# Kernel tuning notes

Hardware: AMD Instinct MI355X
Metric: run time of the kernel (lower is better)

## Reference

```python
import jax, jax.numpy as jnp
import numpy as np

REPLACE = 4
REMAIN = 32
EPS = 1e-12


def _l2norm(x, axis):
    return x / jnp.maximum(jnp.linalg.norm(x, axis=axis, keepdims=True), EPS)


def setup_inputs() -> dict:
    key = jax.random.key(0)
    ks = jax.random.split(key, 16)
    B, d = 4096, 64
    n_users, n_entities, n_items = 100000, 200000, 50000
    K, n_cans, n_rel = 64, 64, 100
    return {
        "users": jax.random.randint(ks[0], (B,), 0, n_users),
        "items": jax.random.randint(ks[1], (B,), 0, n_items),
        "kg_neighbors": jax.random.randint(ks[2], (n_items, K), 0, n_entities),
        "all_candidates": jax.random.randint(ks[3], (n_rel, n_cans), 0, n_entities),
        "neighbor_relations": jax.random.randint(ks[4], (n_items, K), 0, n_rel),
        "user_all_embeddings": jax.random.normal(ks[5], (n_users, d), jnp.float32),
        "entity_all_embeddings": jax.random.normal(ks[6], (n_entities, d), jnp.float32),
        "item_embeddings": jax.random.normal(ks[7], (B, d), jnp.float32),
        "ui_W": jax.random.normal(ks[8], (2 * d, d), jnp.float32) / np.sqrt(2 * d),
        "ui_b": jnp.zeros((d,), jnp.float32),
        "e1_W": jax.random.normal(ks[9], (d, d), jnp.float32) / np.sqrt(d),
        "e1_b": jnp.zeros((d,), jnp.float32),
        "e2_W": jax.random.normal(ks[10], (d, d), jnp.float32) / np.sqrt(d),
        "e2_b": jnp.zeros((d,), jnp.float32),
    }


def reference(users, items, kg_neighbors, all_candidates, neighbor_relations,
              user_all_embeddings, entity_all_embeddings, item_embeddings,
              ui_W, ui_b, e1_W, e1_b, e2_W, e2_b):
    B = users.shape[0]
    d = user_all_embeddings.shape[1]
    idx_dtype = kg_neighbors.dtype

    neighbors = kg_neighbors[items]                      # [B, K]
    users_e = user_all_embeddings[users]                 # [B, d]
    ui_e = _l2norm(jnp.concatenate([users_e, item_embeddings], axis=1) @ ui_W + ui_b, 1)  # [B, d]

    # Step 1: score neighbors, pick top replace_num
    ne = _l2norm(entity_all_embeddings[neighbors] @ e1_W + e1_b, 2)   # [B, K, d]
    scores1 = jnp.einsum('bd,bkd->bk', ui_e, ne)
    logits1 = jax.nn.softmax(scores1, axis=1)
    step1_prob, step1_idx = jax.lax.top_k(logits1, REPLACE)          # [B, R]
    replaced = jnp.take_along_axis(neighbors, step1_idx, axis=1)     # [B, R]
    sel_rel = jnp.take_along_axis(neighbor_relations[items], step1_idx, axis=1)
    cf_kg1 = kg_neighbors.at[items[:, None], step1_idx].set(
        jnp.zeros((B, REPLACE), idx_dtype))
    ap1 = jnp.log(jnp.mean(step1_prob, axis=1))                      # [B]

    # Step 2: candidate pruning + sampling
    cands = all_candidates[sel_rel]                                  # [B, R, C]
    cands_e = entity_all_embeddings[cands]                           # [B, R, C, d]
    scores2 = jnp.einsum('bd,brcd->brc', users_e, cands_e)
    _, remain_idx = jax.lax.top_k(scores2, REMAIN)                   # [B, R, M]
    cands = jnp.take_along_axis(cands, remain_idx, axis=2).reshape(B * REPLACE, REMAIN)

    replaced_e = _l2norm(entity_all_embeddings[replaced] @ e1_W + e1_b, 2)
    replaced_e = replaced_e.reshape(B * REPLACE, d)
    cands_e2 = _l2norm(entity_all_embeddings[cands] @ e2_W + e2_b, 2)  # [BR, M, d]
    ui_rep = jnp.repeat(ui_e, REPLACE, axis=0)                         # [BR, d]
    s2 = jnp.einsum('nd,nmd->nm', ui_rep * replaced_e, cands_e2)       # [BR, M]
    logp2 = jax.nn.log_softmax(s2, axis=1)

    skey = jax.random.key(42)
    step2_idx = jax.random.categorical(skey, logp2, axis=1)           # [BR]
    rows = jnp.arange(B * REPLACE)
    step2_prob = jnp.exp(logp2[rows, step2_idx]).reshape(B, REPLACE)
    sel_ent = cands[rows, step2_idx].reshape(B, REPLACE)
    cf_kg2 = kg_neighbors.at[items[:, None], step1_idx].set(sel_ent.astype(idx_dtype))
    ap2 = jnp.log(jnp.mean(step1_prob, axis=1)) + jnp.log(jnp.mean(step2_prob, axis=1))
    return (cf_kg1, ap1, cf_kg2, ap2)
```

## Files before the change

### kernel.cpp

```cpp
#include <hip/hip_runtime.h>
#include <stdint.h>

#define EPS_NORM 1e-12f
#define F32_TINY 1.17549435e-38f

static __device__ __forceinline__ int rfl(int v) {
  return __builtin_amdgcn_readfirstlane(v);
}

__device__ __forceinline__ void threefry2x32(uint32_t k0, uint32_t k1,
                                             uint32_t x0, uint32_t x1,
                                             uint32_t& o0, uint32_t& o1) {
  uint32_t ks2 = k0 ^ k1 ^ 0x1BD11BDAu;
  x0 += k0; x1 += k1;
#define TF_ROT(r) { x0 += x1; x1 = (x1 << (r)) | (x1 >> (32 - (r))); x1 ^= x0; }
  TF_ROT(13) TF_ROT(15) TF_ROT(26) TF_ROT(6)
  x0 += k1; x1 += ks2 + 1u;
  TF_ROT(17) TF_ROT(29) TF_ROT(16) TF_ROT(24)
  x0 += ks2; x1 += k0 + 2u;
  TF_ROT(13) TF_ROT(15) TF_ROT(26) TF_ROT(6)
  x0 += k0; x1 += k1 + 3u;
  TF_ROT(17) TF_ROT(29) TF_ROT(16) TF_ROT(24)
  x0 += k1; x1 += ks2 + 4u;
  TF_ROT(13) TF_ROT(15) TF_ROT(26) TF_ROT(6)
  x0 += ks2; x1 += k0 + 5u;
#undef TF_ROT
  o0 = x0; o1 = x1;
}

__global__ __launch_bounds__(256) void k_init(const int* __restrict__ kg,
                                              float* __restrict__ out0,
                                              int* __restrict__ wkg2, int n) {
  int i = blockIdx.x * 256 + threadIdx.x;
  if (i < n) { int v = kg[i]; out0[i] = (float)v; wkg2[i] = v; }
}

__device__ __forceinline__ void transform_row(const float4* __restrict__ Er,
                                              const float* __restrict__ W,
                                              const float* __restrict__ bias,
                                              float (&yn)[64]) {
  float y[64];
#pragma unroll
  for (int j = 0; j < 64; ++j) y[j] = 0.f;
  float4 c0 = Er[0], c1 = Er[1], c2 = Er[2], c3 = Er[3];
#pragma unroll 1
  for (int cc = 0; cc < 4; ++cc) {
    float4 n0, n1, n2, n3;
    if (cc < 3) { n0 = Er[cc * 4 + 4]; n1 = Er[cc * 4 + 5];
                  n2 = Er[cc * 4 + 6]; n3 = Er[cc * 4 + 7]; }
    float ev[16] = {c0.x, c0.y, c0.z, c0.w, c1.x, c1.y, c1.z, c1.w,
                    c2.x, c2.y, c2.z, c2.w, c3.x, c3.y, c3.z, c3.w};
#pragma unroll
    for (int k2i = 0; k2i < 16; ++k2i) {
      const float4* Wr = reinterpret_cast<const float4*>(
          W + ((size_t)(cc * 16 + k2i)) * 64);
      float ek = ev[k2i];
#pragma unroll
      for (int j4 = 0; j4 < 16; ++j4) {
        float4 w = Wr[j4];
        y[j4 * 4 + 0] = fmaf(ek, w.x, y[j4 * 4 + 0]);
        y[j4 * 4 + 1] = fmaf(ek, w.y, y[j4 * 4 + 1]);
        y[j4 * 4 + 2] = fmaf(ek, w.z, y[j4 * 4 + 2]);
        y[j4 * 4 + 3] = fmaf(ek, w.w, y[j4 * 4 + 3]);
      }
    }
    c0 = n0; c1 = n1; c2 = n2; c3 = n3;
  }
  const float4* B4 = reinterpret_cast<const float4*>(bias);
#pragma unroll
  for (int j4 = 0; j4 < 16; ++j4) {
    float4 bb = B4[j4];
    float bv[4] = {bb.x, bb.y, bb.z, bb.w};
#pragma unroll
    for (int t = 0; t < 4; ++t) y[j4 * 4 + t] = __fadd_rn(y[j4 * 4 + t], bv[t]);
  }
  float S1[32];
#pragma unroll
  for (int i = 0; i < 32; ++i)
    S1[i] = __fadd_rn(__fmul_rn(y[i], y[i]), __fmul_rn(y[i + 32], y[i + 32]));
#pragma unroll
  for (int i = 0; i < 16; ++i) S1[i] = __fadd_rn(S1[i], S1[i + 16]);
#pragma unroll
  for (int i = 0; i < 8; ++i)  S1[i] = __fadd_rn(S1[i], S1[i + 8]);
#pragma unroll
  for (int i = 0; i < 4; ++i)  S1[i] = __fadd_rn(S1[i], S1[i + 4]);
#pragma unroll
  for (int i = 0; i < 2; ++i)  S1[i] = __fadd_rn(S1[i], S1[i + 2]);
  float ss = __fadd_rn(S1[0], S1[1]);
  float denom = fmaxf(sqrtf(ss), EPS_NORM);
#pragma unroll
  for (int j = 0; j < 64; ++j) yn[j] = y[j] / denom;
}

__global__ __launch_bounds__(256) void k_tx(
    const float* __restrict__ E, const int* __restrict__ allc,
    const float* __restrict__ W1, const float* __restrict__ b1,
    const float* __restrict__ W2, const float* __restrict__ b2,
    float* __restrict__ T1, float* __restrict__ T2c,
    int nEnt , int nCand ) {
  int tid = threadIdx.x, wv = tid >> 6, lane = tid & 63;
  int w = rfl(blockIdx.x * 4 + wv);
  int wEnt = nEnt >> 6;
  int wTot = wEnt + (nCand >> 6);
  if (w >= wTot) return;
  const float *W, *bias; float* dst; int srow, drow;
  if (w < wEnt) { drow = w * 64 + lane; srow = drow; W = W1; bias = b1; dst = T1; }
  else { drow = (w - wEnt) * 64 + lane; srow = allc[drow]; W = W2; bias = b2; dst = T2c; }
  const float4* Er = reinterpret_cast<const float4*>(E + (size_t)srow * 64);
  float yn[64];
  transform_row(Er, W, bias, yn);
  float4* D4 = reinterpret_cast<float4*>(dst + (size_t)drow * 64);
#pragma unroll
  for (int j4 = 0; j4 < 16; ++j4)
    D4[j4] = make_float4(yn[4 * j4], yn[4 * j4 + 1], yn[4 * j4 + 2], yn[4 * j4 + 3]);
}

__global__ __launch_bounds__(256) void k_transform64(
    const float* __restrict__ src, const int* __restrict__ gidx,
    const float* __restrict__ W, const float* __restrict__ bias,
    float* __restrict__ out, int nrows) {
  __shared__ float Wl[4096];
  for (int i = threadIdx.x; i < 4096; i += 256) Wl[i] = W[i];
  __syncthreads();
  int wid = threadIdx.x >> 6, lane = threadIdx.x & 63;
  int row = rfl(blockIdx.x * 4 + wid);
  if (row >= nrows) return;
  int srow = rfl(gidx ? gidx[row] : row);
  const float* er = src + (size_t)srow * 64;
  float y = 0.f;
#pragma unroll
  for (int k = 0; k < 64; ++k) y = fmaf(er[k], Wl[k * 64 + lane], y);
  y += bias[lane];
  float ss = y * y;
#pragma unroll
  for (int off = 32; off; off >>= 1) ss += __shfl_xor(ss, off);
  float yn = y / fmaxf(sqrtf(ss), EPS_NORM);
  out[(size_t)row * 64 + lane] = yn;
}

__global__ __launch_bounds__(256) void k_ui(
    const float* __restrict__ U, const int* __restrict__ users,
    const float* __restrict__ Iemb, const float* __restrict__ W,
    const float* __restrict__ bias, float* __restrict__ out, int B) {
  __shared__ float Wl[8192];
  for (int i = threadIdx.x; i < 8192; i += 256) Wl[i] = W[i];
  __syncthreads();
  int wid = threadIdx.x >> 6, lane = threadIdx.x & 63;
  int b = rfl(blockIdx.x * 4 + wid);
  if (b >= B) return;
  int usr = rfl(users[b]);
  const float* ur = U + (size_t)usr * 64;
  const float* ir = Iemb + (size_t)b * 64;
  float y = 0.f;
#pragma unroll
  for (int k = 0; k < 64; ++k) y = fmaf(ur[k], Wl[k * 64 + lane], y);
#pragma unroll
  for (int k = 0; k < 64; ++k) y = fmaf(ir[k], Wl[(64 + k) * 64 + lane], y);
  y += bias[lane];
  float ss = y * y;
#pragma unroll
  for (int off = 32; off; off >>= 1) ss += __shfl_xor(ss, off);
  float yn = y / fmaxf(sqrtf(ss), EPS_NORM);
  out[(size_t)b * 64 + lane] = yn;
}

__device__ __forceinline__ void score1_tail(
    float s, int lane, int b, int item, int nb,
    const int* __restrict__ nrel,
    float* __restrict__ out0, float* __restrict__ ap1_out,
    int* __restrict__ s1_idx, int* __restrict__ s1_rel, int* __restrict__ s1_ent,
    float* __restrict__ lmp1) {
  float m = s;
#pragma unroll
  for (int off = 32; off; off >>= 1) m = fmaxf(m, __shfl_xor(m, off));
  float ex = expf(s - m);
  float sum = ex;
#pragma unroll
  for (int off = 32; off; off >>= 1) sum += __shfl_xor(sum, off);
  float p = ex / sum;
  int rank = 0;
  for (int k2 = 0; k2 < 64; ++k2) {
    float pv = __shfl(p, k2);
    rank += (pv > p || (pv == p && k2 < lane)) ? 1 : 0;
  }
  float acc = 0.f;
#pragma unroll
  for (int rr = 0; rr < 4; ++rr) {
    unsigned long long msk = __ballot(rank == rr);
    int src = __ffsll(msk) - 1;
    acc += __shfl(p, src);
  }
  float lm = logf(acc * 0.25f);
  if (lane == 0) { ap1_out[b] = lm; lmp1[b] = lm; }
  if (rank < 4) {
    s1_idx[b * 4 + rank] = lane;
    s1_ent[b * 4 + rank] = nb;
    s1_rel[b * 4 + rank] = nrel[(size_t)item * 64 + lane];
    out0[(size_t)item * 64 + lane] = 0.0f;
  }
}

__global__ __launch_bounds__(256) void k_score1g(
    const int* __restrict__ items, const int* __restrict__ kg,
    const int* __restrict__ nrel, const float* __restrict__ T1,
    const float* __restrict__ uiE,
    float* __restrict__ out0, float* __restrict__ ap1_out,
    int* __restrict__ s1_idx, int* __restrict__ s1_rel, int* __restrict__ s1_ent,
    float* __restrict__ lmp1) {
  int tid = threadIdx.x, wv = tid >> 6, lane = tid & 63;
  int b = rfl(blockIdx.x * 4 + wv);
  int item = rfl(items[b]);
  int nb = kg[(size_t)item * 64 + lane];
  const float4* R = reinterpret_cast<const float4*>(T1 + (size_t)nb * 64);
  float yn[64];
#pragma unroll
  for (int j4 = 0; j4 < 16; ++j4) {
    float4 v = R[j4];
    yn[4 * j4] = v.x; yn[4 * j4 + 1] = v.y; yn[4 * j4 + 2] = v.z; yn[4 * j4 + 3] = v.w;
  }
  const float4* Ur = reinterpret_cast<const float4*>(uiE + (size_t)b * 64);
  float D[32];
#pragma unroll
  for (int i4 = 0; i4 < 8; ++i4) {
    float4 ua = Ur[i4], ub = Ur[i4 + 8];
    float uav[4] = {ua.x, ua.y, ua.z, ua.w};
    float ubv[4] = {ub.x, ub.y, ub.z, ub.w};
#pragma unroll
    for (int t = 0; t < 4; ++t) {
      int i = i4 * 4 + t;
      D[i] = __fadd_rn(__fmul_rn(yn[i], uav[t]), __fmul_rn(yn[i + 32], ubv[t]));
    }
  }
#pragma unroll
  for (int i = 0; i < 16; ++i) D[i] = __fadd_rn(D[i], D[i + 16]);
#pragma unroll
  for (int i = 0; i < 8; ++i)  D[i] = __fadd_rn(D[i], D[i + 8]);
#pragma unroll
  for (int i = 0; i < 4; ++i)  D[i] = __fadd_rn(D[i], D[i + 4]);
#pragma unroll
  for (int i = 0; i < 2; ++i)  D[i] = __fadd_rn(D[i], D[i + 2]);
  float s = __fadd_rn(D[0], D[1]);
  score1_tail(s, lane, b, item, nb, nrel, out0, ap1_out, s1_idx, s1_rel, s1_ent, lmp1);
}

__global__ __launch_bounds__(256) void k_score1(
    const int* __restrict__ items, const int* __restrict__ kg,
    const int* __restrict__ nrel, const float* __restrict__ E,
    const float* __restrict__ W1, const float* __restrict__ b1,
    const float* __restrict__ uiE,
    float* __restrict__ out0, float* __restrict__ ap1_out,
    int* __restrict__ s1_idx, int* __restrict__ s1_rel, int* __restrict__ s1_ent,
    float* __restrict__ lmp1) {
  int tid = threadIdx.x, wv = tid >> 6, lane = tid & 63;
  int b = rfl(blockIdx.x * 4 + wv);
  int item = rfl(items[b]);
  int nb = kg[(size_t)item * 64 + lane];
  const float4* Er = reinterpret_cast<const float4*>(E + (size_t)nb * 64);
  float yn[64];
  transform_row(Er, W1, b1, yn);
  const float4* Ur = reinterpret_cast<const float4*>(uiE + (size_t)b * 64);
  float D[32];
#pragma unroll
  for (int i4 = 0; i4 < 8; ++i4) {
    float4 ua = Ur[i4], ub = Ur[i4 + 8];
    float uav[4] = {ua.x, ua.y, ua.z, ua.w};
    float ubv[4] = {ub.x, ub.y, ub.z, ub.w};
#pragma unroll
    for (int t = 0; t < 4; ++t) {
      int i = i4 * 4 + t;
      D[i] = __fadd_rn(__fmul_rn(yn[i], uav[t]), __fmul_rn(yn[i + 32], ubv[t]));
    }
  }
#pragma unroll
  for (int i = 0; i < 16; ++i) D[i] = __fadd_rn(D[i], D[i + 16]);
#pragma unroll
  for (int i = 0; i < 8; ++i)  D[i] = __fadd_rn(D[i], D[i + 8]);
#pragma unroll
  for (int i = 0; i < 4; ++i)  D[i] = __fadd_rn(D[i], D[i + 4]);
#pragma unroll
  for (int i = 0; i < 2; ++i)  D[i] = __fadd_rn(D[i], D[i + 2]);
  float s = __fadd_rn(D[0], D[1]);
  score1_tail(s, lane, b, item, nb, nrel, out0, ap1_out, s1_idx, s1_rel, s1_ent, lmp1);
}

__global__ __launch_bounds__(256) void k_score2(
    const int* __restrict__ users, const int* __restrict__ s1_rel,
    const float* __restrict__ U, const float* __restrict__ E,
    const int* __restrict__ allc, int* __restrict__ kept, int N) {
  int wid = threadIdx.x >> 6, lane = threadIdx.x & 63;
  int n = rfl(blockIdx.x * 4 + wid);
  if (n >= N) return;
  int b = n >> 2;
  int rel = rfl(s1_rel[n]);
  int usr = rfl(users[b]);
  int ent = allc[rel * 64 + lane];
  const float* ur = U + (size_t)usr * 64;
  const float4* e4 = reinterpret_cast<const float4*>(E + (size_t)ent * 64);
  float s = 0.f;
#pragma unroll
  for (int j4 = 0; j4 < 16; ++j4) {
    float4 t = e4[j4];
    s = fmaf(ur[4 * j4 + 0], t.x, s);
    s = fmaf(ur[4 * j4 + 1], t.y, s);
    s = fmaf(ur[4 * j4 + 2], t.z, s);
    s = fmaf(ur[4 * j4 + 3], t.w, s);
  }
  int rank = 0;
  for (int k2 = 0; k2 < 64; ++k2) {
    float sv = __shfl(s, k2);
    rank += (sv > s || (sv == s && k2 < lane)) ? 1 : 0;
  }
  if (rank < 32) kept[n * 32 + rank] = (lane << 18) | ent;
}

__device__ __forceinline__ void sample_body(
    float q, int n, int b, int lane,
    const int* __restrict__ items, const int* __restrict__ s1_idx,
    int rel, const float* __restrict__ T2c, const int* __restrict__ kept,
    float* __restrict__ p2, int* __restrict__ wkg2) {
  int m = lane & 31;
  int pk = kept[n * 32 + m];
  int c = pk >> 18;
  int ent = pk & 0x3FFFF;
  const float4* c4 = reinterpret_cast<const float4*>(T2c + ((size_t)rel * 64 + c) * 64);
  float s = 0.f;
#pragma unroll
  for (int j4 = 0; j4 < 16; ++j4) {
    float4 t = c4[j4];
    s = fmaf(__shfl(q, 4 * j4 + 0), t.x, s);
    s = fmaf(__shfl(q, 4 * j4 + 1), t.y, s);
    s = fmaf(__shfl(q, 4 * j4 + 2), t.z, s);
    s = fmaf(__shfl(q, 4 * j4 + 3), t.w, s);
  }
  float mx = s;
#pragma unroll
  for (int off = 1; off < 32; off <<= 1) mx = fmaxf(mx, __shfl_xor(mx, off));
  float shv = s - mx;
  float se = expf(shv);
  float sum = se;
#pragma unroll
  for (int off = 1; off < 32; off <<= 1) sum += __shfl_xor(sum, off);
  float logp = shv - logf(sum);
  uint32_t h0, h1;
  threefry2x32(0u, 42u, 0u, (uint32_t)(n * 32 + m), h0, h1);
  uint32_t bits = h0 ^ h1;
  float u0 = __uint_as_float((bits >> 9) | 0x3F800000u) - 1.0f;
  float uu = fmaxf(u0, F32_TINY);
  float g = -logf(-logf(uu));
  float z = g + logp;
  float bz = z; int bm = m;
#pragma unroll
  for (int off = 1; off < 32; off <<= 1) {
    float oz = __shfl_xor(bz, off);
    int om = __shfl_xor(bm, off);
    if (oz > bz || (oz == bz && om < bm)) { bz = oz; bm = om; }
  }
  if (lane == bm) {
    p2[n] = expf(logp);
    int col = s1_idx[n];
    int item = items[b];
    atomicMax(&wkg2[(size_t)item * 64 + col], ((b + 1) << 18) | ent);
  }
}

__global__ __launch_bounds__(256) void k_sample2(
    const int* __restrict__ items,
    const int* __restrict__ s1_idx, const int* __restrict__ s1_rel,
    const int* __restrict__ s1_ent, const float* __restrict__ T1,
    const float* __restrict__ T2c, const float* __restrict__ uiE,
    const int* __restrict__ kept,
    float* __restrict__ p2, int* __restrict__ wkg2, int N) {
  int tid = threadIdx.x, wid = tid >> 6, lane = tid & 63;
  int n = rfl(blockIdx.x * 4 + wid);
  if (n >= N) return;
  int b = n >> 2;
  int rel = rfl(s1_rel[n]);
  int repl = rfl(s1_ent[n]);
  float q = uiE[(size_t)b * 64 + lane] * T1[(size_t)repl * 64 + lane];
  sample_body(q, n, b, lane, items, s1_idx, rel, T2c, kept, p2, wkg2);
}

__global__ __launch_bounds__(256) void k_sample(
    const int* __restrict__ items,
    const int* __restrict__ s1_idx, const int* __restrict__ s1_rel,
    const int* __restrict__ s1_ent,
    const float* __restrict__ E, const float* __restrict__ W1,
    const float* __restrict__ b1, const float* __restrict__ T2c,
    const float* __restrict__ uiE, const int* __restrict__ kept,
    float* __restrict__ p2, int* __restrict__ wkg2, int N) {
  __shared__ float Wl[4096];
  int tid = threadIdx.x;
  for (int i = tid; i < 4096; i += 256) Wl[i] = W1[i];
  __syncthreads();
  int wid = tid >> 6, lane = tid & 63;
  int n = rfl(blockIdx.x * 4 + wid);
  if (n >= N) return;
  int b = n >> 2;
  int rel = rfl(s1_rel[n]);
  int repl = rfl(s1_ent[n]);
  const float* er = E + (size_t)repl * 64;
  float y = 0.f;
#pragma unroll
  for (int k2 = 0; k2 < 64; ++k2) y = fmaf(er[k2], Wl[k2 * 64 + lane], y);
  y += b1[lane];
  float ss = y * y;
#pragma unroll
  for (int off = 32; off; off >>= 1) ss += __shfl_xor(ss, off);
  float yn = y / fmaxf(sqrtf(ss), EPS_NORM);
  float q = uiE[(size_t)b * 64 + lane] * yn;
  sample_body(q, n, b, lane, items, s1_idx, rel, T2c, kept, p2, wkg2);
}

__global__ __launch_bounds__(256) void k_fin(const int* __restrict__ wkg2,
                                             const float* __restrict__ p2,
                                             const float* __restrict__ lmp1,
                                             float* __restrict__ out2,
                                             float* __restrict__ out3,
                                             int n, int B) {
  int i = blockIdx.x * 256 + threadIdx.x;
  if (i < n) out2[i] = (float)(wkg2[i] & 0x3FFFF);
  if (i < B) {
    float a = ((p2[i * 4] + p2[i * 4 + 1]) + p2[i * 4 + 2]) + p2[i * 4 + 3];
    out3[i] = lmp1[i] + logf(a * 0.25f);
  }
}

extern "C" void kernel_launch(void* const* d_in, const int* in_sizes, int n_in,
                              void* d_out, int out_size, void* d_ws, size_t ws_size,
                              hipStream_t stream) {
  const int*   users = (const int*)d_in[0];
  const int*   items = (const int*)d_in[1];
  const int*   kg    = (const int*)d_in[2];
  const int*   allc  = (const int*)d_in[3];
  const int*   nrel  = (const int*)d_in[4];
  const float* U     = (const float*)d_in[5];
  const float* E     = (const float*)d_in[6];
  const float* Iemb  = (const float*)d_in[7];
  const float* uiW   = (const float*)d_in[8];
  const float* uib   = (const float*)d_in[9];
  const float* e1W   = (const float*)d_in[10];
  const float* e1b   = (const float*)d_in[11];
  const float* e2W   = (const float*)d_in[12];
  const float* e2b   = (const float*)d_in[13];

  const int B = 4096, NCELL = 3200000, NCAND = 6400, NR4 = 16384, NENT = 200000;

  float* out0    = (float*)d_out;
  float* out_ap1 = out0 + NCELL;
  float* out2    = out_ap1 + B;
  float* out_ap2 = out2 + NCELL;

  float* T2c  = (float*)d_ws;
  float* uiE  = T2c + 409600;
  int*   wkg2 = (int*)(uiE + 262144);
  int*   s1i  = wkg2 + NCELL;
  int*   s1r  = s1i + NR4;
  int*   s1e  = s1r + NR4;
  int*   kept = s1e + NR4;
  float* p2   = (float*)(kept + 524288);
  float* lmp1 = p2 + NR4;
  float* T1   = lmp1 + B;
  const size_t WS_NEED = ((size_t)(T1 + (size_t)NENT * 64) - (size_t)d_ws);
  const bool pathA = ws_size >= WS_NEED;

  k_init<<<(NCELL + 255) / 256, 256, 0, stream>>>(kg, out0, wkg2, NCELL);
  k_ui<<<(B + 3) / 4, 256, 0, stream>>>(U, users, Iemb, uiW, uib, uiE, B);
  if (pathA) {
    int wTot = (NENT >> 6) + (NCAND >> 6);
    k_tx<<<(wTot + 3) / 4, 256, 0, stream>>>(E, allc, e1W, e1b, e2W, e2b,
                                             T1, T2c, NENT, NCAND);
    k_score1g<<<B / 4, 256, 0, stream>>>(items, kg, nrel, T1, uiE,
                                         out0, out_ap1, s1i, s1r, s1e, lmp1);
    k_score2<<<(NR4 + 3) / 4, 256, 0, stream>>>(users, s1r, U, E, allc, kept, NR4);
    k_sample2<<<(NR4 + 3) / 4, 256, 0, stream>>>(items, s1i, s1r, s1e, T1, T2c,
                                                 uiE, kept, p2, wkg2, NR4);
  } else {
    k_transform64<<<(NCAND + 3) / 4, 256, 0, stream>>>(E, allc, e2W, e2b, T2c, NCAND);
    k_score1<<<B / 4, 256, 0, stream>>>(items, kg, nrel, E, e1W, e1b, uiE,
                                        out0, out_ap1, s1i, s1r, s1e, lmp1);
    k_score2<<<(NR4 + 3) / 4, 256, 0, stream>>>(users, s1r, U, E, allc, kept, NR4);
    k_sample<<<(NR4 + 3) / 4, 256, 0, stream>>>(items, s1i, s1r, s1e, E, e1W, e1b,
                                                T2c, uiE, kept, p2, wkg2, NR4);
  }
  k_fin<<<(NCELL + 255) / 256, 256, 0, stream>>>(wkg2, p2, lmp1, out2, out_ap2,
                                                 NCELL, B);
}
```

Before: 158.6 us.

## Fuse init, ui, and entity transforms into one phase-1 kernel

Merges k_init, k_ui and k_tx into a single k_phase1 launch whose blocks are partitioned by role. The entity transform now stages W in LDS and has each lane compute one output column for four rows per pass, with a wave-shuffle norm, instead of one row per lane held in registers. The candidate embeddings are also gathered into a compact buffer (borrowed from the out2 region) so score2 reads them contiguously. The intent is fewer launches, lower register pressure and better memory locality, at the cost of fixed hardcoded block counts and reusing the output buffer as scratch.

```diff
diff --git a/kernel.cpp b/kernel.cpp
--- a/kernel.cpp
+++ b/kernel.cpp
@@ -28,6 +28,98 @@
   o0 = x0; o1 = x1;
 }
 
+__global__ __launch_bounds__(256) void k_phase1(
+    const float* __restrict__ E, const int* __restrict__ allc,
+    const float* __restrict__ W1, const float* __restrict__ b1,
+    const float* __restrict__ W2, const float* __restrict__ b2,
+    const float* __restrict__ U, const int* __restrict__ users,
+    const float* __restrict__ Iemb, const float* __restrict__ uiW,
+    const float* __restrict__ uib, const int* __restrict__ kg,
+    float* __restrict__ T1, float* __restrict__ T2c, float* __restrict__ Eg,
+    float* __restrict__ uiE, float* __restrict__ out0, int* __restrict__ wkg2) {
+  __shared__ float Wl[4096];
+  const int blk = blockIdx.x, tid = threadIdx.x;
+  const int wv = tid >> 6, lane = tid & 63;
+  if (blk < 807) {
+    const bool isT1 = blk < 782;
+    const float* W = isT1 ? W1 : W2;
+    const float* bias = isT1 ? b1 : b2;
+    for (int i = tid; i < 4096; i += 256) Wl[i] = W[i];
+    __syncthreads();
+    int w = isT1 ? blk * 4 + wv : (blk - 782) * 4 + wv;
+    if (isT1 && w >= 3125) return;
+    float bl = bias[lane];
+    float* dst = isT1 ? T1 : T2c;
+    const int rbase = w * 64;
+#pragma unroll 1
+    for (int pass = 0; pass < 16; ++pass) {
+      int r0 = rbase + pass * 4;
+      int sr0, sr1, sr2, sr3;
+      if (isT1) { sr0 = r0; sr1 = r0 + 1; sr2 = r0 + 2; sr3 = r0 + 3; }
+      else {
+        sr0 = rfl(allc[r0]);     sr1 = rfl(allc[r0 + 1]);
+        sr2 = rfl(allc[r0 + 2]); sr3 = rfl(allc[r0 + 3]);
+      }
+      const float* e0 = E + (size_t)sr0 * 64;
+      const float* e1 = E + (size_t)sr1 * 64;
+      const float* e2 = E + (size_t)sr2 * 64;
+      const float* e3 = E + (size_t)sr3 * 64;
+      float y0 = 0.f, y1 = 0.f, y2 = 0.f, y3 = 0.f;
+#pragma unroll
+      for (int k = 0; k < 64; ++k) {
+        float wk = Wl[k * 64 + lane];
+        y0 = fmaf(e0[k], wk, y0);
+        y1 = fmaf(e1[k], wk, y1);
+        y2 = fmaf(e2[k], wk, y2);
+        y3 = fmaf(e3[k], wk, y3);
+      }
+      y0 += bl; y1 += bl; y2 += bl; y3 += bl;
+      float ys[4] = {y0, y1, y2, y3};
+#pragma unroll
+      for (int q = 0; q < 4; ++q) {
+        float y = ys[q];
+        float ss = y * y;
+#pragma unroll
+        for (int off = 32; off; off >>= 1) ss += __shfl_xor(ss, off);
+        float yn = y / fmaxf(sqrtf(ss), EPS_NORM);
+        dst[(size_t)(r0 + q) * 64 + lane] = yn;
+      }
+      if (!isT1) {
+        Eg[(size_t)r0 * 64 + lane]       = e0[lane];
+        Eg[(size_t)(r0 + 1) * 64 + lane] = e1[lane];
+        Eg[(size_t)(r0 + 2) * 64 + lane] = e2[lane];
+        Eg[(size_t)(r0 + 3) * 64 + lane] = e3[lane];
+      }
+    }
+  } else if (blk < 1063) {
+    int ib = blk - 807;
+    const int4* kg4 = reinterpret_cast<const int4*>(kg);
+    float4* o4 = reinterpret_cast<float4*>(out0);
+    int4* w4 = reinterpret_cast<int4*>(wkg2);
+    for (int i = ib * 256 + tid; i < 800000; i += 256 * 256) {
+      int4 v = kg4[i];
+      o4[i] = make_float4((float)v.x, (float)v.y, (float)v.z, (float)v.w);
+      w4[i] = v;
+    }
+  } else {
+    int b = (blk - 1063) * 4 + wv;
+    int usr = rfl(users[b]);
+    const float* ur = U + (size_t)usr * 64;
+    const float* ir = Iemb + (size_t)b * 64;
+    float y = 0.f;
+#pragma unroll
+    for (int k = 0; k < 64; ++k) y = fmaf(ur[k], uiW[k * 64 + lane], y);
+#pragma unroll
+    for (int k = 0; k < 64; ++k) y = fmaf(ir[k], uiW[(64 + k) * 64 + lane], y);
+    y += uib[lane];
+    float ss = y * y;
+#pragma unroll
+    for (int off = 32; off; off >>= 1) ss += __shfl_xor(ss, off);
+    float yn = y / fmaxf(sqrtf(ss), EPS_NORM);
+    uiE[(size_t)b * 64 + lane] = yn;
+  }
+}
+
 __global__ __launch_bounds__(256) void k_init(const int* __restrict__ kg,
                                               float* __restrict__ out0,
                                               int* __restrict__ wkg2, int n) {
@@ -90,29 +182,6 @@
   float denom = fmaxf(sqrtf(ss), EPS_NORM);
 #pragma unroll
   for (int j = 0; j < 64; ++j) yn[j] = y[j] / denom;
-}
-
-__global__ __launch_bounds__(256) void k_tx(
-    const float* __restrict__ E, const int* __restrict__ allc,
-    const float* __restrict__ W1, const float* __restrict__ b1,
-    const float* __restrict__ W2, const float* __restrict__ b2,
-    float* __restrict__ T1, float* __restrict__ T2c,
-    int nEnt , int nCand ) {
-  int tid = threadIdx.x, wv = tid >> 6, lane = tid & 63;
-  int w = rfl(blockIdx.x * 4 + wv);
-  int wEnt = nEnt >> 6;
-  int wTot = wEnt + (nCand >> 6);
-  if (w >= wTot) return;
-  const float *W, *bias; float* dst; int srow, drow;
-  if (w < wEnt) { drow = w * 64 + lane; srow = drow; W = W1; bias = b1; dst = T1; }
-  else { drow = (w - wEnt) * 64 + lane; srow = allc[drow]; W = W2; bias = b2; dst = T2c; }
-  const float4* Er = reinterpret_cast<const float4*>(E + (size_t)srow * 64);
-  float yn[64];
-  transform_row(Er, W, bias, yn);
-  float4* D4 = reinterpret_cast<float4*>(dst + (size_t)drow * 64);
-#pragma unroll
-  for (int j4 = 0; j4 < 16; ++j4)
-    D4[j4] = make_float4(yn[4 * j4], yn[4 * j4 + 1], yn[4 * j4 + 2], yn[4 * j4 + 3]);
 }
 
 __global__ __launch_bounds__(256) void k_transform64(
@@ -281,6 +350,36 @@
   for (int i = 0; i < 2; ++i)  D[i] = __fadd_rn(D[i], D[i + 2]);
   float s = __fadd_rn(D[0], D[1]);
   score1_tail(s, lane, b, item, nb, nrel, out0, ap1_out, s1_idx, s1_rel, s1_ent, lmp1);
+}
+
+__global__ __launch_bounds__(256) void k_score2e(
+    const int* __restrict__ users, const int* __restrict__ s1_rel,
+    const float* __restrict__ U, const float* __restrict__ Eg,
+    const int* __restrict__ allc, int* __restrict__ kept, int N) {
+  int wid = threadIdx.x >> 6, lane = threadIdx.x & 63;
+  int n = rfl(blockIdx.x * 4 + wid);
+  if (n >= N) return;
+  int b = n >> 2;
+  int rel = rfl(s1_rel[n]);
+  int usr = rfl(users[b]);
+  int ent = allc[rel * 64 + lane];
+  const float* ur = U + (size_t)usr * 64;
+  const float4* e4 = reinterpret_cast<const float4*>(Eg + ((size_t)rel * 64 + lane) * 64);
+  float s = 0.f;
+#pragma unroll
+  for (int j4 = 0; j4 < 16; ++j4) {
+    float4 t = e4[j4];
+    s = fmaf(ur[4 * j4 + 0], t.x, s);
+    s = fmaf(ur[4 * j4 + 1], t.y, s);
+    s = fmaf(ur[4 * j4 + 2], t.z, s);
+    s = fmaf(ur[4 * j4 + 3], t.w, s);
+  }
+  int rank = 0;
+  for (int k2 = 0; k2 < 64; ++k2) {
+    float sv = __shfl(s, k2);
+    rank += (sv > s || (sv == s && k2 < lane)) ? 1 : 0;
+  }
+  if (rank < 32) kept[n * 32 + rank] = (lane << 18) | ent;
 }
 
 __global__ __launch_bounds__(256) void k_score2(
@@ -460,21 +559,22 @@
   float* p2   = (float*)(kept + 524288);
   float* lmp1 = p2 + NR4;
   float* T1   = lmp1 + B;
+  float* Eg   = out2;
   const size_t WS_NEED = ((size_t)(T1 + (size_t)NENT * 64) - (size_t)d_ws);
   const bool pathA = ws_size >= WS_NEED;
 
-  k_init<<<(NCELL + 255) / 256, 256, 0, stream>>>(kg, out0, wkg2, NCELL);
-  k_ui<<<(B + 3) / 4, 256, 0, stream>>>(U, users, Iemb, uiW, uib, uiE, B);
   if (pathA) {
-    int wTot = (NENT >> 6) + (NCAND >> 6);
-    k_tx<<<(wTot + 3) / 4, 256, 0, stream>>>(E, allc, e1W, e1b, e2W, e2b,
-                                             T1, T2c, NENT, NCAND);
+    k_phase1<<<2087, 256, 0, stream>>>(E, allc, e1W, e1b, e2W, e2b, U, users,
+                                       Iemb, uiW, uib, kg, T1, T2c, Eg, uiE,
+                                       out0, wkg2);
     k_score1g<<<B / 4, 256, 0, stream>>>(items, kg, nrel, T1, uiE,
                                          out0, out_ap1, s1i, s1r, s1e, lmp1);
-    k_score2<<<(NR4 + 3) / 4, 256, 0, stream>>>(users, s1r, U, E, allc, kept, NR4);
+    k_score2e<<<(NR4 + 3) / 4, 256, 0, stream>>>(users, s1r, U, Eg, allc, kept, NR4);
     k_sample2<<<(NR4 + 3) / 4, 256, 0, stream>>>(items, s1i, s1r, s1e, T1, T2c,
                                                  uiE, kept, p2, wkg2, NR4);
   } else {
+    k_init<<<(NCELL + 255) / 256, 256, 0, stream>>>(kg, out0, wkg2, NCELL);
+    k_ui<<<(B + 3) / 4, 256, 0, stream>>>(U, users, Iemb, uiW, uib, uiE, B);
     k_transform64<<<(NCAND + 3) / 4, 256, 0, stream>>>(E, allc, e2W, e2b, T2c, NCAND);
     k_score1<<<B / 4, 256, 0, stream>>>(items, kg, nrel, E, e1W, e1b, uiE,
                                         out0, out_ap1, s1i, s1r, s1e, lmp1);
```

After: 269.4 us. 69.9% more time.
